# Optimization experiments

Hardware: AMD Instinct MI355X
Metric: run time of the kernel (lower is better)

The kernel has to match this reference:

```python
import jax, jax.numpy as jnp
import numpy as np

EMBED_DIM = 512
FFN_DIM = 2048
N_QUBITS = 8
BATCH = 16
SEQ = 2048


def setup_inputs() -> dict:
    key = jax.random.key(0)
    k_x, k_t, k_w1, k_w2 = jax.random.split(key, 4)
    x = jax.random.normal(k_x, (BATCH, SEQ, EMBED_DIM), dtype=jnp.float32)
    # per-wire trainable RX angles (nn.Parameter(torch.randn(1)) per qubit)
    theta = jax.random.normal(k_t, (N_QUBITS,), dtype=jnp.float32)
    # nn.Linear weights, bias=False; stored as [out, in] like torch
    s1 = 1.0 / np.sqrt(N_QUBITS)
    s2 = 1.0 / np.sqrt(FFN_DIM)
    W1 = jax.random.uniform(k_w1, (FFN_DIM, N_QUBITS), jnp.float32, -s1, s1)
    W2 = jax.random.uniform(k_w2, (EMBED_DIM, FFN_DIM), jnp.float32, -s2, s2)
    return {"x": x, "theta": theta, "W1": W1, "W2": W2}


def reference(x, theta, W1, W2):
    # Quantum circuit closed form: each wire i gets RX(x_i) twice (outer loop
    # + encoder) plus trainable RX(theta_i); product state => <Z_i> = cos(total angle).
    q = jnp.cos(2.0 * x[..., :N_QUBITS] + theta)          # [B, S, n_qubits]
    # dropout in eval mode is identity
    h = jax.nn.relu(jnp.einsum('bsq,fq->bsf', q, W1))     # [B, S, ffn_dim]
    out = jnp.einsum('bsf,ef->bse', h, W2)                # [B, S, embed_dim]
    return out
```

## Files before the change

kernel.cpp:

```cpp
#include <hip/hip_runtime.h>
#include <cstdint>

#define BATCH 16
#define SEQ 2048
#define EMB 512
#define FFN 2048
#define NQ 8
#define M_TOTAL (BATCH * SEQ)

#define BM 128
#define BN 256
#define BK 32
#define NTHREADS 256

typedef __attribute__((ext_vector_type(8))) short short8;
typedef __attribute__((ext_vector_type(4))) float float4v;
typedef __attribute__((ext_vector_type(4))) unsigned int uint4v;

static __device__ __forceinline__ unsigned int f2bf(float f) {
    unsigned int u = __builtin_bit_cast(unsigned int, f);
    return (u + 0x7fffu + ((u >> 16) & 1u)) >> 16;
}
static __device__ __forceinline__ unsigned int f2bf_pk(float lo, float hi) {
    return f2bf(lo) | (f2bf(hi) << 16);
}
static __device__ __forceinline__ unsigned int cvt_pk_bf16(float lo, float hi) {
    unsigned int r;
    asm("v_cvt_pk_bf16_f32 %0, %1, %2" : "=v"(r) : "v"(lo), "v"(hi));
    return r;
}

__global__ __launch_bounds__(256) void prep_w2(const float* __restrict__ W2,
                                               unsigned int* __restrict__ w2b) {
    int idx = (blockIdx.x * 256 + threadIdx.x) * 4;
    float4 v = *(const float4*)&W2[idx];
    w2b[idx / 2]     = f2bf_pk(v.x, v.y);
    w2b[idx / 2 + 1] = f2bf_pk(v.z, v.w);
}


__global__ __launch_bounds__(NTHREADS, 2) void ffq_main(
    const float* __restrict__ x,
    const float* __restrict__ theta,
    const unsigned short* __restrict__ w1b,
    const unsigned short* __restrict__ w2b,
    float* __restrict__ out)
{
    __shared__ unsigned short Asm[2][BM * BK];
    __shared__ unsigned short Bsm[2][BN * BK];

    const int t    = threadIdx.x;
    const int m0   = blockIdx.x * BM;
    const int n0   = blockIdx.y * BN;
    const int wave = t >> 6, lane = t & 63;
    const int quad = lane >> 4, l16 = lane & 15;
    const int wm   = wave >> 1, wn = wave & 1;

    short8 qfrag[2];
#pragma unroll
    for (int g2 = 0; g2 < 2; ++g2) {
        int qrow = m0 + wave * 32 + g2 * 16 + l16;
        const float* xr = x + (size_t)qrow * EMB;
        float4 xa = *(const float4*)xr;
        float4 xb = *(const float4*)(xr + 4);
        uint4v uq;
        uq[0] = f2bf_pk(__cosf(2.f * xa.x + theta[0]), __cosf(2.f * xa.y + theta[1]));
        uq[1] = f2bf_pk(__cosf(2.f * xa.z + theta[2]), __cosf(2.f * xa.w + theta[3]));
        uq[2] = f2bf_pk(__cosf(2.f * xb.x + theta[4]), __cosf(2.f * xb.y + theta[5]));
        uq[3] = f2bf_pk(__cosf(2.f * xb.z + theta[6]), __cosf(2.f * xb.w + theta[7]));
        qfrag[g2] = __builtin_bit_cast(short8, uq);
        if (quad != 0) qfrag[g2] = (short8)0;
    }

    const unsigned short* gB[4];
#pragma unroll
    for (int i = 0; i < 4; ++i) {
        int c = i * NTHREADS + t;
        int n = c >> 2, s = c & 3;
        gB[i] = w2b + (size_t)(n0 + n) * FFN + (s ^ ((n >> 1) & 3)) * 8;
    }

    auto stageB = [&](int k0, int buf) __attribute__((always_inline)) {
#pragma unroll
        for (int i = 0; i < 4; ++i) {
            int c = i * NTHREADS + t;
            __builtin_amdgcn_global_load_lds(
                (const __attribute__((address_space(1))) unsigned int*)(gB[i] + k0),
                (__attribute__((address_space(3))) unsigned int*)(uintptr_t)(&Bsm[buf][c * 8]),
                16, 0, 0);
        }
    };

    auto loadW1 = [&](int kh, short8& a, short8& b) __attribute__((always_inline)) {
        a = *(const short8*)&w1b[(size_t)(kh + l16) * NQ];
        b = *(const short8*)&w1b[(size_t)(kh + 16 + l16) * NQ];
    };

    const int hswz = (l16 >> 1) & 3;
    auto hgen = [&](int buf, short8 w1f0, short8 w1f1) __attribute__((always_inline)) {
#pragma unroll
        for (int g2 = 0; g2 < 2; ++g2) {
#pragma unroll
            for (int fh = 0; fh < 2; ++fh) {
                float4v hc = __builtin_amdgcn_mfma_f32_16x16x32_bf16(
                    fh ? w1f1 : w1f0, qfrag[g2], (float4v)0.0f, 0, 0, 0);
                unsigned int p0 = cvt_pk_bf16(fmaxf(hc[0], 0.f), fmaxf(hc[1], 0.f));
                unsigned int p1 = cvt_pk_bf16(fmaxf(hc[2], 0.f), fmaxf(hc[3], 0.f));
                int m   = wave * 32 + g2 * 16 + l16;
                int qph = (fh * 2 + (quad >> 1)) ^ hswz;
                unsigned long long pk = ((unsigned long long)p1 << 32) | p0;
                *(unsigned long long*)&Asm[buf][m * 32 + qph * 8 + (quad & 1) * 4] = pk;
            }
        }
    };

    float4v acc[32];
#pragma unroll
    for (int i = 0; i < 32; ++i) acc[i] = (float4v)0.0f;

    auto compute = [&](int buf) __attribute__((always_inline)) {
        short8 af[4], bfr[8];
#pragma unroll
        for (int fm = 0; fm < 4; ++fm) {
            int row = wm * 64 + fm * 16 + l16;
            int qph = quad ^ ((row >> 1) & 3);
            af[fm] = *(const short8*)&Asm[buf][row * 32 + qph * 8];
        }
#pragma unroll
        for (int fn = 0; fn < 8; ++fn) {
            int row = wn * 128 + fn * 16 + l16;
            int qph = quad ^ ((row >> 1) & 3);
            bfr[fn] = *(const short8*)&Bsm[buf][row * 32 + qph * 8];
        }
        __builtin_amdgcn_s_setprio(1);
#pragma unroll
        for (int fm = 0; fm < 4; ++fm)
#pragma unroll
            for (int fn = 0; fn < 8; ++fn)
                acc[fm * 8 + fn] = __builtin_amdgcn_mfma_f32_16x16x32_bf16(
                    af[fm], bfr[fn], acc[fm * 8 + fn], 0, 0, 0);
        __builtin_amdgcn_s_setprio(0);
    };

    {
        short8 w1f0, w1f1;
        loadW1(0, w1f0, w1f1);
        stageB(0, 0);
        hgen(0, w1f0, w1f1);
    }
    __syncthreads();

    for (int kt = 0; kt < 62; kt += 2) {
        {
            short8 w1f0, w1f1;
            loadW1((kt + 1) * BK, w1f0, w1f1);
            stageB((kt + 1) * BK, 1);
            compute(0);
            hgen(1, w1f0, w1f1);
        }
        __syncthreads();
        {
            short8 w1f0, w1f1;
            loadW1((kt + 2) * BK, w1f0, w1f1);
            stageB((kt + 2) * BK, 0);
            compute(1);
            hgen(0, w1f0, w1f1);
        }
        __syncthreads();
    }
    {
        short8 w1f0, w1f1;
        loadW1(63 * BK, w1f0, w1f1);
        stageB(63 * BK, 1);
        compute(0);
        hgen(1, w1f0, w1f1);
    }
    __syncthreads();
    compute(1);

    const int om = m0 + wm * 64;
    const int on = n0 + wn * 128;
#pragma unroll
    for (int fm = 0; fm < 4; ++fm) {
#pragma unroll
        for (int fn = 0; fn < 8; ++fn) {
            float4v v = acc[fm * 8 + fn];
            int rbase = om + fm * 16 + quad * 4;
            int c     = on + fn * 16 + l16;
#pragma unroll
            for (int r = 0; r < 4; ++r)
                out[(size_t)(rbase + r) * EMB + c] = v[r];
        }
    }
}

extern "C" void kernel_launch(void* const* d_in, const int* in_sizes, int n_in,
                              void* d_out, int out_size, void* d_ws, size_t ws_size,
                              hipStream_t stream) {
    const float* x     = (const float*)d_in[0];
    const float* theta = (const float*)d_in[1];
    const float* W1    = (const float*)d_in[2];
    const float* W2    = (const float*)d_in[3];
    float* out = (float*)d_out;

    unsigned int* w2b = (unsigned int*)d_ws;
    unsigned int* w1b = (unsigned int*)((char*)d_ws + (size_t)EMB * FFN * 2);

    prep_w2<<<(EMB * FFN) / (256 * 4), 256, 0, stream>>>(W2, w2b);
    prep_w2<<<(FFN * NQ) / (256 * 4), 256, 0, stream>>>(W1, w1b);

    dim3 grid(M_TOTAL / BM, EMB / BN);
    ffq_main<<<grid, NTHREADS, 0, stream>>>(x, theta,
                                            (const unsigned short*)w1b,
                                            (const unsigned short*)w2b, out);
}
```

Before: 173.4 us.

## Keep hidden activations in registers via 32x32 MFMA layout, drop A shared-memory staging

Switches both GEMM stages to 32x32x16 bf16 MFMA. W1 rows are permuted in a new prep kernel so that the output layout of the first MFMA matches the A-operand layout the second MFMA expects. The ReLU'd hidden tile therefore stays in registers, and the Asm shared-memory buffer and its writes and reads go away. Each wave now recomputes its own hidden fragments (redundantly across the wn waves), trading some extra MFMA work and a different output store pattern for less LDS traffic.

```diff
diff --git a/kernel.cpp b/kernel.cpp
--- a/kernel.cpp
+++ b/kernel.cpp
@@ -14,7 +14,7 @@
 #define NTHREADS 256
 
 typedef __attribute__((ext_vector_type(8))) short short8;
-typedef __attribute__((ext_vector_type(4))) float float4v;
+typedef __attribute__((ext_vector_type(16))) float float16v;
 typedef __attribute__((ext_vector_type(4))) unsigned int uint4v;
 
 static __device__ __forceinline__ unsigned int f2bf(float f) {
@@ -38,28 +38,41 @@
     w2b[idx / 2 + 1] = f2bf_pk(v.z, v.w);
 }
 
+__global__ __launch_bounds__(256) void prep_w1(const float* __restrict__ W1,
+                                               unsigned int* __restrict__ w1p) {
+    int row = blockIdx.x * 256 + threadIdx.x;
+    int g = (row >> 2) & 7;
+    int off = ((g & 3) == 1) ? 4 : ((g & 3) == 2) ? -4 : 0;
+    const float* s = &W1[(row + off) * NQ];
+    float4 a = *(const float4*)s;
+    float4 b = *(const float4*)(s + 4);
+    w1p[row * 4 + 0] = f2bf_pk(a.x, a.y);
+    w1p[row * 4 + 1] = f2bf_pk(a.z, a.w);
+    w1p[row * 4 + 2] = f2bf_pk(b.x, b.y);
+    w1p[row * 4 + 3] = f2bf_pk(b.z, b.w);
+}
+
 
 __global__ __launch_bounds__(NTHREADS, 2) void ffq_main(
     const float* __restrict__ x,
     const float* __restrict__ theta,
-    const unsigned short* __restrict__ w1b,
+    const unsigned short* __restrict__ w1p,
     const unsigned short* __restrict__ w2b,
     float* __restrict__ out)
 {
-    __shared__ unsigned short Asm[2][BM * BK];
     __shared__ unsigned short Bsm[2][BN * BK];
 
     const int t    = threadIdx.x;
     const int m0   = blockIdx.x * BM;
     const int n0   = blockIdx.y * BN;
     const int wave = t >> 6, lane = t & 63;
-    const int quad = lane >> 4, l16 = lane & 15;
+    const int l32  = lane & 31, hi = lane >> 5;
     const int wm   = wave >> 1, wn = wave & 1;
 
     short8 qfrag[2];
 #pragma unroll
-    for (int g2 = 0; g2 < 2; ++g2) {
-        int qrow = m0 + wave * 32 + g2 * 16 + l16;
+    for (int mh = 0; mh < 2; ++mh) {
+        int qrow = m0 + wm * 64 + mh * 32 + l32;
         const float* xr = x + (size_t)qrow * EMB;
         float4 xa = *(const float4*)xr;
         float4 xb = *(const float4*)(xr + 4);
@@ -68,8 +81,8 @@
         uq[1] = f2bf_pk(__cosf(2.f * xa.z + theta[2]), __cosf(2.f * xa.w + theta[3]));
         uq[2] = f2bf_pk(__cosf(2.f * xb.x + theta[4]), __cosf(2.f * xb.y + theta[5]));
         uq[3] = f2bf_pk(__cosf(2.f * xb.z + theta[6]), __cosf(2.f * xb.w + theta[7]));
-        qfrag[g2] = __builtin_bit_cast(short8, uq);
-        if (quad != 0) qfrag[g2] = (short8)0;
+        qfrag[mh] = __builtin_bit_cast(short8, uq);
+        if (hi) qfrag[mh] = (short8)0;
     }
 
     const unsigned short* gB[4];
@@ -91,105 +104,92 @@
         }
     };
 
-    auto loadW1 = [&](int kh, short8& a, short8& b) __attribute__((always_inline)) {
-        a = *(const short8*)&w1b[(size_t)(kh + l16) * NQ];
-        b = *(const short8*)&w1b[(size_t)(kh + 16 + l16) * NQ];
-    };
-
-    const int hswz = (l16 >> 1) & 3;
-    auto hgen = [&](int buf, short8 w1f0, short8 w1f1) __attribute__((always_inline)) {
-#pragma unroll
-        for (int g2 = 0; g2 < 2; ++g2) {
-#pragma unroll
-            for (int fh = 0; fh < 2; ++fh) {
-                float4v hc = __builtin_amdgcn_mfma_f32_16x16x32_bf16(
-                    fh ? w1f1 : w1f0, qfrag[g2], (float4v)0.0f, 0, 0, 0);
-                unsigned int p0 = cvt_pk_bf16(fmaxf(hc[0], 0.f), fmaxf(hc[1], 0.f));
-                unsigned int p1 = cvt_pk_bf16(fmaxf(hc[2], 0.f), fmaxf(hc[3], 0.f));
-                int m   = wave * 32 + g2 * 16 + l16;
-                int qph = (fh * 2 + (quad >> 1)) ^ hswz;
-                unsigned long long pk = ((unsigned long long)p1 << 32) | p0;
-                *(unsigned long long*)&Asm[buf][m * 32 + qph * 8 + (quad & 1) * 4] = pk;
+    auto loadW1 = [&](int k) __attribute__((always_inline)) -> short8 {
+        short8 w = (short8)0;
+        if (hi == 0) w = *(const short8*)&w1p[(size_t)(k + l32) * NQ];
+        return w;
+    };
+
+    float16v acc[2][4];
+#pragma unroll
+    for (int mh = 0; mh < 2; ++mh)
+#pragma unroll
+        for (int nh = 0; nh < 4; ++nh) acc[mh][nh] = (float16v)0.0f;
+
+    short8 af[2][2];
+    auto hgen = [&](short8 w1f) __attribute__((always_inline)) {
+#pragma unroll
+        for (int mh = 0; mh < 2; ++mh) {
+            float16v hc = __builtin_amdgcn_mfma_f32_32x32x16_bf16(
+                w1f, qfrag[mh], (float16v)0.0f, 0, 0, 0);
+            unsigned int d[8];
+#pragma unroll
+            for (int r = 0; r < 8; ++r)
+                d[r] = cvt_pk_bf16(fmaxf(hc[2 * r], 0.f), fmaxf(hc[2 * r + 1], 0.f));
+            uint4v u0, u1;
+            u0[0] = d[0]; u0[1] = d[1]; u0[2] = d[2]; u0[3] = d[3];
+            u1[0] = d[4]; u1[1] = d[5]; u1[2] = d[6]; u1[3] = d[7];
+            af[mh][0] = __builtin_bit_cast(short8, u0);
+            af[mh][1] = __builtin_bit_cast(short8, u1);
+        }
+    };
+
+    auto mainC = [&](int buf) __attribute__((always_inline)) {
+        __builtin_amdgcn_s_setprio(1);
+#pragma unroll
+        for (int nh = 0; nh < 4; ++nh) {
+            int row = wn * 128 + nh * 32 + l32;
+            int sw  = (row >> 1) & 3;
+            short8 b0 = *(const short8*)&Bsm[buf][row * BK + ((hi)     ^ sw) * 8];
+            short8 b1 = *(const short8*)&Bsm[buf][row * BK + ((2 + hi) ^ sw) * 8];
+#pragma unroll
+            for (int mh = 0; mh < 2; ++mh) {
+                acc[mh][nh] = __builtin_amdgcn_mfma_f32_32x32x16_bf16(
+                    af[mh][0], b0, acc[mh][nh], 0, 0, 0);
+                acc[mh][nh] = __builtin_amdgcn_mfma_f32_32x32x16_bf16(
+                    af[mh][1], b1, acc[mh][nh], 0, 0, 0);
             }
         }
-    };
-
-    float4v acc[32];
-#pragma unroll
-    for (int i = 0; i < 32; ++i) acc[i] = (float4v)0.0f;
-
-    auto compute = [&](int buf) __attribute__((always_inline)) {
-        short8 af[4], bfr[8];
-#pragma unroll
-        for (int fm = 0; fm < 4; ++fm) {
-            int row = wm * 64 + fm * 16 + l16;
-            int qph = quad ^ ((row >> 1) & 3);
-            af[fm] = *(const short8*)&Asm[buf][row * 32 + qph * 8];
-        }
-#pragma unroll
-        for (int fn = 0; fn < 8; ++fn) {
-            int row = wn * 128 + fn * 16 + l16;
-            int qph = quad ^ ((row >> 1) & 3);
-            bfr[fn] = *(const short8*)&Bsm[buf][row * 32 + qph * 8];
-        }
-        __builtin_amdgcn_s_setprio(1);
-#pragma unroll
-        for (int fm = 0; fm < 4; ++fm)
-#pragma unroll
-            for (int fn = 0; fn < 8; ++fn)
-                acc[fm * 8 + fn] = __builtin_amdgcn_mfma_f32_16x16x32_bf16(
-                    af[fm], bfr[fn], acc[fm * 8 + fn], 0, 0, 0);
         __builtin_amdgcn_s_setprio(0);
     };
 
-    {
-        short8 w1f0, w1f1;
-        loadW1(0, w1f0, w1f1);
-        stageB(0, 0);
-        hgen(0, w1f0, w1f1);
-    }
+    short8 wA = loadW1(0), wB;
+    stageB(0, 0);
     __syncthreads();
 
     for (int kt = 0; kt < 62; kt += 2) {
-        {
-            short8 w1f0, w1f1;
-            loadW1((kt + 1) * BK, w1f0, w1f1);
-            stageB((kt + 1) * BK, 1);
-            compute(0);
-            hgen(1, w1f0, w1f1);
-        }
+        wB = loadW1((kt + 1) * BK);
+        stageB((kt + 1) * BK, 1);
+        hgen(wA);
+        mainC(0);
         __syncthreads();
-        {
-            short8 w1f0, w1f1;
-            loadW1((kt + 2) * BK, w1f0, w1f1);
-            stageB((kt + 2) * BK, 0);
-            compute(1);
-            hgen(0, w1f0, w1f1);
-        }
+
+        wA = loadW1((kt + 2) * BK);
+        stageB((kt + 2) * BK, 0);
+        hgen(wB);
+        mainC(1);
         __syncthreads();
     }
-    {
-        short8 w1f0, w1f1;
-        loadW1(63 * BK, w1f0, w1f1);
-        stageB(63 * BK, 1);
-        compute(0);
-        hgen(1, w1f0, w1f1);
-    }
+    wB = loadW1(63 * BK);
+    stageB(63 * BK, 1);
+    hgen(wA);
+    mainC(0);
     __syncthreads();
-    compute(1);
-
-    const int om = m0 + wm * 64;
-    const int on = n0 + wn * 128;
-#pragma unroll
-    for (int fm = 0; fm < 4; ++fm) {
-#pragma unroll
-        for (int fn = 0; fn < 8; ++fn) {
-            float4v v = acc[fm * 8 + fn];
-            int rbase = om + fm * 16 + quad * 4;
-            int c     = on + fn * 16 + l16;
-#pragma unroll
-            for (int r = 0; r < 4; ++r)
-                out[(size_t)(rbase + r) * EMB + c] = v[r];
+    hgen(wB);
+    mainC(1);
+
+#pragma unroll
+    for (int mh = 0; mh < 2; ++mh) {
+#pragma unroll
+        for (int nh = 0; nh < 4; ++nh) {
+            float16v v = acc[mh][nh];
+            int n  = n0 + wn * 128 + nh * 32 + l32;
+            int mb = m0 + wm * 64 + mh * 32 + 4 * hi;
+#pragma unroll
+            for (int r = 0; r < 16; ++r) {
+                int m = mb + (r & 3) + 8 * (r >> 2);
+                out[(size_t)m * EMB + n] = v[r];
+            }
         }
     }
 }
@@ -204,13 +204,13 @@
     float* out = (float*)d_out;
 
     unsigned int* w2b = (unsigned int*)d_ws;
-    unsigned int* w1b = (unsigned int*)((char*)d_ws + (size_t)EMB * FFN * 2);
+    unsigned int* w1p = (unsigned int*)((char*)d_ws + (size_t)EMB * FFN * 2);
 
     prep_w2<<<(EMB * FFN) / (256 * 4), 256, 0, stream>>>(W2, w2b);
-    prep_w2<<<(FFN * NQ) / (256 * 4), 256, 0, stream>>>(W1, w1b);
+    prep_w1<<<FFN / 256, 256, 0, stream>>>(W1, w1p);
 
     dim3 grid(M_TOTAL / BM, EMB / BN);
     ffq_main<<<grid, NTHREADS, 0, stream>>>(x, theta,
-                                            (const unsigned short*)w1b,
+                                            (const unsigned short*)w1p,
                                             (const unsigned short*)w2b, out);
 }
```

After: 182.1 us. 1.05x slower.
